# Optimization experiments

Hardware: AMD Instinct MI355X
Metric: run time of the kernel (lower is better)

The kernel has to match this reference:

```python
import jax, jax.numpy as jnp
import numpy as np
import math

# dims
B, T, HFEAT, E = 32, 8, 128, 128
NUM_CLS, NUM_GLOBAL = 4, 2
NSP = NUM_CLS + NUM_GLOBAL            # 6 special tokens
SCALES = (1, 4, 8)
WINDOW = 4
NHEAD = 8
DH = E // NHEAD                        # 16
NLAYERS = 2                            # blocks per scale = ceil(6/3)
NS = len(SCALES)
F = 512                                # dim_feedforward
ROPE_BASE = 100000.0
NEG = -1e9


def setup_inputs() -> dict:
    key = jax.random.key(0)
    ks = jax.random.split(key, 16)
    def rn(k, shape, s=0.02):
        return jax.random.normal(k, shape, jnp.float32) * s
    inp = {
        'embeddings': jax.random.normal(ks[0], (B, T, NSP + HFEAT, E), jnp.float32),
        'cls_tokens': rn(ks[1], (NUM_CLS, E)),
        'global_tokens': rn(ks[2], (NUM_GLOBAL, E)),
        'Wq': rn(ks[3], (NS, NLAYERS, E, E)),
        'bq': jnp.zeros((NS, NLAYERS, E), jnp.float32),
        'Wk': rn(ks[4], (NS, NLAYERS, E, E)),
        'bk': jnp.zeros((NS, NLAYERS, E), jnp.float32),
        'Wv': rn(ks[5], (NS, NLAYERS, E, E)),
        'bv': jnp.zeros((NS, NLAYERS, E), jnp.float32),
        'Wo': rn(ks[6], (NS, NLAYERS, E, E)),
        'bo': jnp.zeros((NS, NLAYERS, E), jnp.float32),
        'ln1_g': jnp.ones((NS, NLAYERS, E), jnp.float32),
        'ln1_b': jnp.zeros((NS, NLAYERS, E), jnp.float32),
        'ln2_g': jnp.ones((NS, NLAYERS, E), jnp.float32),
        'ln2_b': jnp.zeros((NS, NLAYERS, E), jnp.float32),
        'W1': rn(ks[7], (NS, NLAYERS, E, F)),
        'b1': jnp.zeros((NS, NLAYERS, F), jnp.float32),
        'W2': rn(ks[8], (NS, NLAYERS, F, E)),
        'b2': jnp.zeros((NS, NLAYERS, E), jnp.float32),
        'out_g': jnp.ones((E,), jnp.float32),
        'out_b': jnp.zeros((E,), jnp.float32),
    }
    return inp


def _layernorm(x, g, b, eps=1e-5):
    mu = x.mean(-1, keepdims=True)
    var = ((x - mu) ** 2).mean(-1, keepdims=True)
    return (x - mu) * jax.lax.rsqrt(var + eps) * g + b


def _rope(x):
    # x: (BT, L, H, DH); rotate-half RoPE over head dim
    L = x.shape[1]
    half = DH // 2
    inv = ROPE_BASE ** (-jnp.arange(half, dtype=jnp.float32) / half)
    ang = jnp.arange(L, dtype=jnp.float32)[:, None] * inv[None, :]   # (L, half)
    cos = jnp.cos(ang)[None, :, None, :]
    sin = jnp.sin(ang)[None, :, None, :]
    x1, x2 = x[..., :half], x[..., half:]
    return jnp.concatenate([x1 * cos - x2 * sin, x1 * sin + x2 * cos], axis=-1)


def _sparse_bias(L):
    # global(first NSP) rows/cols fully connected, others window +-WINDOW, diag allowed
    i = jnp.arange(L)
    allowed = (jnp.abs(i[:, None] - i[None, :]) <= WINDOW) | (i[:, None] < NSP) | (i[None, :] < NSP)
    return jnp.where(allowed, 0.0, NEG).astype(jnp.float32)  # (L, L) additive


def _encoder(x, s, Wq, bq, Wk, bk, Wv, bv, Wo, bo, ln1_g, ln1_b, ln2_g, ln2_b, W1, b1, W2, b2, bias):
    # x: (BT, L, E); pre-norm transformer encoder with RoPE attention
    BT, L, _ = x.shape
    for l in range(NLAYERS):
        h = _layernorm(x, ln1_g[s, l], ln1_b[s, l])
        q = (h @ Wq[s, l] + bq[s, l]).reshape(BT, L, NHEAD, DH)
        k = (h @ Wk[s, l] + bk[s, l]).reshape(BT, L, NHEAD, DH)
        v = (h @ Wv[s, l] + bv[s, l]).reshape(BT, L, NHEAD, DH)
        q, k = _rope(q), _rope(k)
        scores = jnp.einsum('blhd,bmhd->bhlm', q, k) / math.sqrt(DH) + bias[None, None]
        attn = jax.nn.softmax(scores, axis=-1)
        o = jnp.einsum('bhlm,bmhd->blhd', attn, v).reshape(BT, L, E)
        x = x + o @ Wo[s, l] + bo[s, l]
        h2 = _layernorm(x, ln2_g[s, l], ln2_b[s, l])
        x = x + jax.nn.gelu(h2 @ W1[s, l] + b1[s, l]) @ W2[s, l] + b2[s, l]
    return x


def reference(embeddings, cls_tokens, global_tokens, Wq, bq, Wk, bk, Wv, bv, Wo, bo,
              ln1_g, ln1_b, ln2_g, ln2_b, W1, b1, W2, b2, out_g, out_b):
    Bb, Tt, HC, Ee = embeddings.shape
    feats = embeddings[..., NSP:, :]                                 # (B,T,H,E)
    specials = jnp.broadcast_to(
        jnp.concatenate([cls_tokens, global_tokens], axis=0)[None, None],
        (Bb, Tt, NSP, Ee))
    cls_per_scale = []
    for s, g in enumerate(SCALES):
        H = feats.shape[2]
        K = H // g  # H divisible by all scales
        grouped = feats.reshape(Bb, Tt, K, g, Ee).mean(axis=3)       # contiguous mean grouping
        seq = jnp.concatenate([specials, grouped], axis=2)           # (B,T,L,E)
        L = NSP + K
        x = seq.reshape(Bb * Tt, L, Ee)
        bias = _sparse_bias(L)
        out = _encoder(x, s, Wq, bq, Wk, bk, Wv, bv, Wo, bo,
                       ln1_g, ln1_b, ln2_g, ln2_b, W1, b1, W2, b2, bias)
        cls_per_scale.append(out.reshape(Bb, Tt, L, Ee)[..., :NUM_CLS, :])
    cls_out = jnp.stack(cls_per_scale, axis=0).mean(axis=0)          # (B,T,num_cls,E)
    cls_out = _layernorm(cls_out, out_g, out_b)
    return cls_out.reshape(Bb, Tt, NUM_CLS * Ee)
```

## Files before the change

kernel.cpp:

```cpp
#include <hip/hip_runtime.h>
#include <hip/hip_bf16.h>

#define BT     256
#define EDIM   128
#define NSP    6
#define RT     49664
#define O1     34304
#define O2     44032
#define KSTR   20

typedef unsigned short u16;
typedef short s16x8 __attribute__((ext_vector_type(8)));
typedef float f32x4 __attribute__((ext_vector_type(4)));

__device__ __forceinline__ float u2f(u16 u){ union{unsigned i; float f;} v; v.i=((unsigned)u)<<16; return v.f; }
__device__ __forceinline__ u16 f2u(float f){
  union{float f; unsigned i;} v; v.f = f;
  unsigned r = v.i + 0x7FFF + ((v.i >> 16) & 1);
  return (u16)(r >> 16);
}
__device__ __forceinline__ float ldin(const void* p, size_t idx, int flag){
  return flag ? u2f(((const u16*)p)[idx]) : ((const float*)p)[idx];
}
__device__ __forceinline__ void unp8(uint4 v, float* f){
  f[0]=u2f((u16)(v.x)); f[1]=u2f((u16)(v.x>>16));
  f[2]=u2f((u16)(v.y)); f[3]=u2f((u16)(v.y>>16));
  f[4]=u2f((u16)(v.z)); f[5]=u2f((u16)(v.z>>16));
  f[6]=u2f((u16)(v.w)); f[7]=u2f((u16)(v.w>>16));
}

__device__ __forceinline__ void rowinfo(int row, int& s, int& r, int& L, int& g){
  if (row < O1){ s=0; r=row;    L=134; g=1; }
  else if (row < O2){ s=1; r=row-O1; L=38; g=4; }
  else { s=2; r=row-O2; L=22; g=8; }
}

__device__ __forceinline__ float gelu_f(float x){
  float u = x*(1.5957691216f + 0.0713548162f*x*x);
  return x * __builtin_amdgcn_rcpf(1.f + __expf(-u));
}

__global__ void detect_k(const void* ln1g, int* flagp){
  unsigned v = *(const unsigned*)ln1g;
  *flagp = (v == 0x3F803F80u) ? 1 : 0;
}

struct CArg { const void* src; unsigned dstoff; unsigned n; unsigned inblk; unsigned outblk; };
struct CArgs { CArg a[12]; };
__global__ __launch_bounds__(256) void conv_k(CArgs ca, u16* stage, const int* flagp){
  int i = blockIdx.y;
  int flag = *flagp;
  const CArg& c = ca.a[i];
  for (unsigned idx = blockIdx.x*256u + threadIdx.x; idx < c.n; idx += gridDim.x*256u){
    unsigned blk = idx / c.inblk, r = idx % c.inblk;
    float v = flag ? u2f(((const u16*)c.src)[idx]) : ((const float*)c.src)[idx];
    stage[c.dstoff + blk*c.outblk + r] = flag ? ((const u16*)c.src)[idx] : f2u(v);
  }
}

__global__ __launch_bounds__(256) void convw_k(const void* s0, const void* s1, const void* s2,
                                               u16* dst, int K, int N, int Nsrc, const int* flagp)
{
  int flag = *flagp;
  const void* srcs[3] = {s0, s1, s2};
  int total = 6 * K * N;
  for (int idx = blockIdx.x*256 + threadIdx.x; idx < total; idx += gridDim.x*256) {
    int blk = idx / (K*N);
    int rem = idx % (K*N);
    int j = rem & 7;
    int t = rem >> 3;
    int n = t % N;
    int ck = t / N;
    int k = ck*8 + j;
    int w = n / Nsrc;
    int nn = n - w*Nsrc;
    size_t sidx = (size_t)blk*K*Nsrc + (size_t)k*Nsrc + nn;
    dst[idx] = flag ? ((const u16*)srcs[w])[sidx] : f2u(((const float*)srcs[w])[sidx]);
  }
}

__global__ __launch_bounds__(128) void build_k(const void* __restrict__ emb,
                                               const void* __restrict__ cls,
                                               const void* __restrict__ glob,
                                               float* __restrict__ x,
                                               u16* __restrict__ H,
                                               const u16* __restrict__ lnG,
                                               const u16* __restrict__ lnB,
                                               const int* flagp)
{
  __shared__ float red[4];
  int flag = *flagp;
  int row = blockIdx.x, e = threadIdx.x;
  int s, r, L, g; rowinfo(row, s, r, L, g);
  int seq = r / L, pos = r % L;
  float val;
  if (pos < NSP) {
    val = (pos < 4) ? ldin(cls, pos*EDIM + e, flag) : ldin(glob, (pos-4)*EDIM + e, flag);
  } else {
    int k = pos - NSP;
    size_t base = ((size_t)seq*134 + NSP + (size_t)k*g)*EDIM + e;
    float sum = 0.f;
    for (int j = 0; j < g; j++) sum += ldin(emb, base + (size_t)j*EDIM, flag);
    val = sum / (float)g;
  }
  x[(size_t)row*EDIM + e] = val;
  int wid = e >> 6;
  float sum = val, ss = val*val;
  #pragma unroll
  for (int off = 32; off; off >>= 1) { sum += __shfl_xor(sum, off); ss += __shfl_xor(ss, off); }
  if ((e & 63) == 0) { red[wid] = sum; red[2+wid] = ss; }
  __syncthreads();
  float ts = red[0]+red[1], tss = red[2]+red[3];
  float mu = ts * (1.f/128.f);
  float var = tss * (1.f/128.f) - mu*mu;
  float rs = rsqrtf(var + 1e-5f);
  const u16* gp = lnG + s*2*EDIM;
  const u16* bp = lnB + s*2*EDIM;
  H[(size_t)row*EDIM + e] = f2u((val-mu)*rs*u2f(gp[e]) + u2f(bp[e]));
}

template<int EPI>
__global__ __launch_bounds__(256) void gemm64_k(
    const u16* __restrict__ A,
    const u16* __restrict__ Wt, const u16* __restrict__ Bias,
    u16* __restrict__ C, int ldc, int N, int layer,
    float* __restrict__ X, u16* __restrict__ H,
    const u16* __restrict__ lnG, const u16* __restrict__ lnB, int lnidx)
{
  __shared__ u16 As[4][16*136];
  __shared__ u16 Bs[16*128*8];
  const int row0 = blockIdx.x * 64;
  const int n0 = blockIdx.y * 128;
  const int s = row0 < O1 ? 0 : (row0 < O2 ? 1 : 2);
  const u16* Wp = Wt + (size_t)(s*2+layer)*128*N;
  const u16* bp = Bias + (size_t)(s*2+layer)*N + n0;
  const int tid = threadIdx.x;
  const int lane = tid & 63, w = tid >> 6;
  const int g = lane >> 4, l15 = lane & 15;

  #pragma unroll
  for (int i = 0; i < 4; i++) {
    int unit = lane + i*64;
    int r = unit >> 4, kc = unit & 15;
    *(uint4*)&As[w][r*136 + kc*8] = *(const uint4*)(A + (size_t)(row0 + w*16 + r)*128 + kc*8);
  }
  #pragma unroll
  for (int i = 0; i < 8; i++) {
    int u = tid + i*256;
    int kb = u >> 7, nn = u & 127;
    *(uint4*)&Bs[u*8] = *(const uint4*)(Wp + ((size_t)kb*N + n0 + nn)*8);
  }
  __syncthreads();

  f32x4 acc[8];
  #pragma unroll
  for (int nt = 0; nt < 8; nt++) acc[nt] = (f32x4){0.f,0.f,0.f,0.f};
  #pragma unroll
  for (int ks = 0; ks < 4; ks++) {
    int c = ks*4 + g;
    s16x8 af = *(const s16x8*)&As[w][l15*136 + c*8];
    #pragma unroll
    for (int nt = 0; nt < 8; nt++) {
      s16x8 bf = *(const s16x8*)&Bs[(c*128 + nt*16 + l15)*8];
      acc[nt] = __builtin_amdgcn_mfma_f32_16x16x32_bf16(af, bf, acc[nt], 0, 0, 0);
    }
  }

  float bb[8];
  #pragma unroll
  for (int nt = 0; nt < 8; nt++) bb[nt] = u2f(bp[nt*16 + l15]);

  #pragma unroll
  for (int reg = 0; reg < 4; reg++) {
    int row = row0 + w*16 + g*4 + reg;
    #pragma unroll
    for (int nt = 0; nt < 8; nt++)
      C[(size_t)row*ldc + n0 + nt*16 + l15] = f2u(acc[nt][reg] + bb[nt]);
  }
}

template<int LNFUSE>
__global__ __launch_bounds__(256, 3) void woffn_k(
    const u16* __restrict__ A,
    const u16* __restrict__ Wot, const u16* __restrict__ Bo,
    const u16* __restrict__ W1t, const u16* __restrict__ B1,
    const u16* __restrict__ W2t, const u16* __restrict__ B2,
    float* __restrict__ X,
    u16* __restrict__ H,
    const u16* __restrict__ ln2G, const u16* __restrict__ ln2B,
    const u16* __restrict__ ln1G, const u16* __restrict__ ln1B,
    int layer)
{
  __shared__ u16 Hs[4][16*136];
  __shared__ u16 Ts[2][4][16*40];
  const int row0 = blockIdx.x * 64;
  const int s = row0 < O1 ? 0 : (row0 < O2 ? 1 : 2);
  const int sl = s*2 + layer;
  const u16* Wop = Wot + (size_t)sl*16384;
  const u16* bop = Bo  + sl*128;
  const u16* W1p = W1t + (size_t)sl*65536;
  const u16* b1p = B1  + sl*512;
  const u16* W2p = W2t + (size_t)sl*65536;
  const u16* b2p = B2  + sl*128;
  const int tid = threadIdx.x;
  const int lane = tid & 63, w = tid >> 6;
  const int g = lane >> 4, l15 = lane & 15;

  s16x8 af[4];
  {
    const u16* arow = A + (size_t)(row0 + w*16 + l15)*128;
    #pragma unroll
    for (int ks = 0; ks < 4; ks++) af[ks] = *(const s16x8*)(arow + (ks*4 + g)*8);
  }
  const u16* wobase = Wop + ((size_t)g*128 + l15)*8;

  f32x4 acc2[8];
  #pragma unroll
  for (int nt = 0; nt < 8; nt++) acc2[nt] = (f32x4){0.f,0.f,0.f,0.f};
  #pragma unroll
  for (int ks = 0; ks < 4; ks++) {
    s16x8 bw[8];
    #pragma unroll
    for (int nt = 0; nt < 8; nt++)
      bw[nt] = *(const s16x8*)(wobase + ((size_t)ks*4096 + nt*128));
    #pragma unroll
    for (int nt = 0; nt < 8; nt++)
      acc2[nt] = __builtin_amdgcn_mfma_f32_16x16x32_bf16(af[ks], bw[nt], acc2[nt], 0, 0, 0);
  }

  {
    float gam[8], bet[8], bo_[8];
    const u16* gp  = ln2G + sl*EDIM;
    const u16* bp2 = ln2B + sl*EDIM;
    #pragma unroll
    for (int nt = 0; nt < 8; nt++) {
      gam[nt] = u2f(gp[nt*16+l15]); bet[nt] = u2f(bp2[nt*16+l15]);
      bo_[nt] = u2f(bop[nt*16+l15]);
    }
    #pragma unroll
    for (int reg = 0; reg < 4; reg++) {
      int row = row0 + w*16 + g*4 + reg;
      float vals[8], ps = 0.f, pss = 0.f;
      #pragma unroll
      for (int nt = 0; nt < 8; nt++) {
        float v = acc2[nt][reg] + bo_[nt] + X[(size_t)row*128 + nt*16 + l15];
        vals[nt] = v; ps += v; pss += v*v;
      }
      #pragma unroll
      for (int off = 1; off < 16; off <<= 1) { ps += __shfl_xor(ps, off); pss += __shfl_xor(pss, off); }
      float mu = ps * (1.f/128.f);
      float var = pss * (1.f/128.f) - mu*mu;
      float rs = rsqrtf(var + 1e-5f);
      #pragma unroll
      for (int nt = 0; nt < 8; nt++) {
        acc2[nt][reg] = vals[nt];
        Hs[w][(g*4+reg)*136 + nt*16 + l15] = f2u((vals[nt]-mu)*rs*gam[nt] + bet[nt]);
      }
    }
  }

  s16x8 hf[4];
  #pragma unroll
  for (int ks = 0; ks < 4; ks++) hf[ks] = *(const s16x8*)&Hs[w][l15*136 + (ks*4+g)*8];

  const u16* w1base = W1p + ((size_t)g*512 + l15)*8;
  const u16* w2base = W2p + ((size_t)g*128 + l15)*8;

  s16x8 bw1[8];
  #pragma unroll
  for (int ks = 0; ks < 4; ks++)
    #pragma unroll
    for (int nt = 0; nt < 2; nt++)
      bw1[ks*2+nt] = *(const s16x8*)(w1base + (size_t)(ks*2048 + nt*16)*8);

  {
    f32x4 acc1[2];
    acc1[0] = (f32x4){0.f,0.f,0.f,0.f};
    acc1[1] = (f32x4){0.f,0.f,0.f,0.f};
    #pragma unroll
    for (int ks = 0; ks < 4; ks++) {
      acc1[0] = __builtin_amdgcn_mfma_f32_16x16x32_bf16(hf[ks], bw1[ks*2+0], acc1[0], 0, 0, 0);
      acc1[1] = __builtin_amdgcn_mfma_f32_16x16x32_bf16(hf[ks], bw1[ks*2+1], acc1[1], 0, 0, 0);
    }
    #pragma unroll
    for (int ks = 0; ks < 4; ks++)
      #pragma unroll
      for (int nt = 0; nt < 2; nt++)
        bw1[ks*2+nt] = *(const s16x8*)(w1base + (size_t)(ks*2048 + 32 + nt*16)*8);
    #pragma unroll
    for (int nt = 0; nt < 2; nt++) {
      float bb1 = u2f(b1p[nt*16 + l15]);
      #pragma unroll
      for (int reg = 0; reg < 4; reg++)
        Ts[0][w][(g*4+reg)*40 + nt*16 + l15] = f2u(gelu_f(acc1[nt][reg] + bb1));
    }
  }

  for (int i = 1; i < 16; i++) {
    const int f0 = i*32, fp = f0 - 32;
    u16* tsC = &Ts[i & 1][w][0];
    const u16* tsP = &Ts[(i & 1) ^ 1][w][0];

    s16x8 bw2a[4];
    #pragma unroll
    for (int nt = 0; nt < 4; nt++)
      bw2a[nt] = *(const s16x8*)(w2base + (size_t)(fp*16 + nt*16)*8);
    s16x8 af2p = *(const s16x8*)(tsP + l15*40 + g*8);

    f32x4 acc1[2];
    acc1[0] = (f32x4){0.f,0.f,0.f,0.f};
    acc1[1] = (f32x4){0.f,0.f,0.f,0.f};
    #pragma unroll
    for (int ks = 0; ks < 4; ks++) {
      acc1[0] = __builtin_amdgcn_mfma_f32_16x16x32_bf16(hf[ks], bw1[ks*2+0], acc1[0], 0, 0, 0);
      acc1[1] = __builtin_amdgcn_mfma_f32_16x16x32_bf16(hf[ks], bw1[ks*2+1], acc1[1], 0, 0, 0);
    }
    {
      const int fn = (f0 + 32) & 511;
      #pragma unroll
      for (int ks = 0; ks < 4; ks++)
        #pragma unroll
        for (int nt = 0; nt < 2; nt++)
          bw1[ks*2+nt] = *(const s16x8*)(w1base + (size_t)(ks*2048 + fn + nt*16)*8);
    }
    s16x8 bw2b[4];
    #pragma unroll
    for (int nt = 0; nt < 4; nt++)
      bw2b[nt] = *(const s16x8*)(w2base + (size_t)(fp*16 + 64 + nt*16)*8);

    #pragma unroll
    for (int nt = 0; nt < 2; nt++) {
      float bb1 = u2f(b1p[f0 + nt*16 + l15]);
      #pragma unroll
      for (int reg = 0; reg < 4; reg++)
        tsC[(g*4+reg)*40 + nt*16 + l15] = f2u(gelu_f(acc1[nt][reg] + bb1));
    }

    #pragma unroll
    for (int nt = 0; nt < 4; nt++)
      acc2[nt] = __builtin_amdgcn_mfma_f32_16x16x32_bf16(af2p, bw2a[nt], acc2[nt], 0, 0, 0);
    #pragma unroll
    for (int nt = 0; nt < 4; nt++)
      acc2[4+nt] = __builtin_amdgcn_mfma_f32_16x16x32_bf16(af2p, bw2b[nt], acc2[4+nt], 0, 0, 0);
  }

  {
    s16x8 af2p = *(const s16x8*)&Ts[1][w][l15*40 + g*8];
    #pragma unroll
    for (int nt = 0; nt < 8; nt++) {
      s16x8 b = *(const s16x8*)(w2base + (size_t)(480*16 + nt*16)*8);
      acc2[nt] = __builtin_amdgcn_mfma_f32_16x16x32_bf16(af2p, b, acc2[nt], 0, 0, 0);
    }
  }

  float bb2[8];
  #pragma unroll
  for (int nt = 0; nt < 8; nt++) bb2[nt] = u2f(b2p[nt*16 + l15]);

  if (LNFUSE) {
    float gam[8], bet[8];
    const u16* gp  = ln1G + (s*2+1)*EDIM;
    const u16* bpn = ln1B + (s*2+1)*EDIM;
    #pragma unroll
    for (int nt = 0; nt < 8; nt++) { gam[nt] = u2f(gp[nt*16+l15]); bet[nt] = u2f(bpn[nt*16+l15]); }
    #pragma unroll
    for (int reg = 0; reg < 4; reg++) {
      int row = row0 + w*16 + g*4 + reg;
      float vals[8], ps = 0.f, pss = 0.f;
      #pragma unroll
      for (int nt = 0; nt < 8; nt++) {
        float v = acc2[nt][reg] + bb2[nt];
        vals[nt] = v; ps += v; pss += v*v;
      }
      #pragma unroll
      for (int off = 1; off < 16; off <<= 1) { ps += __shfl_xor(ps, off); pss += __shfl_xor(pss, off); }
      float mu = ps * (1.f/128.f);
      float var = pss * (1.f/128.f) - mu*mu;
      float rs = rsqrtf(var + 1e-5f);
      #pragma unroll
      for (int nt = 0; nt < 8; nt++) {
        size_t cidx = (size_t)row*128 + nt*16 + l15;
        X[cidx] = vals[nt];
        H[cidx] = f2u((vals[nt]-mu)*rs*gam[nt] + bet[nt]);
      }
    }
  } else {
    #pragma unroll
    for (int reg = 0; reg < 4; reg++) {
      int row = row0 + w*16 + g*4 + reg;
      #pragma unroll
      for (int nt = 0; nt < 8; nt++) {
        size_t cidx = (size_t)row*128 + nt*16 + l15;
        X[cidx] = acc2[nt][reg] + bb2[nt];
      }
    }
  }
}

__global__ __launch_bounds__(128) void attn_k(const u16* __restrict__ qkv, u16* __restrict__ o)
{
  __shared__ float Ks[134*KSTR];
  __shared__ float Vs[134*KSTR];
  int gseq = blockIdx.x, hd = blockIdx.y;
  int L, base;
  if (gseq < 256)      { L = 134; base = gseq*134; }
  else if (gseq < 512) { L = 38;  base = O1 + (gseq-256)*38; }
  else                 { L = 22;  base = O2 + (gseq-512)*22; }
  int tid = threadIdx.x;
  for (int u = tid; u < L*2; u += 128) {
    int kv = u & 1, row = u >> 1;
    const u16* p = qkv + (size_t)(base+row)*384 + 128 + kv*128 + hd*16;
    uint4 w0 = *(const uint4*)p, w1 = *(const uint4*)(p+8);
    float f[16];
    unp8(w0, f); unp8(w1, f+8);
    if (kv == 0) {
      #pragma unroll
      for (int d = 0; d < 8; d++) {
        float inv = __expf(-(float)d * (11.512925465f/8.f));
        float ang = (float)row * inv;
        float cs = __cosf(ang), sn = __sinf(ang);
        float a = f[d], b = f[d+8];
        f[d]   = a*cs - b*sn;
        f[d+8] = a*sn + b*cs;
      }
    }
    float* dst = (kv ? Vs : Ks) + row*KSTR;
    #pragma unroll
    for (int d = 0; d < 16; d++) dst[d] = f[d];
  }
  __syncthreads();

  for (int it = tid; it < L - NSP; it += 128) {
    int row = NSP + it;
    const u16* qp = qkv + (size_t)(base+row)*384 + hd*16;
    uint4 w0 = *(const uint4*)qp, w1 = *(const uint4*)(qp+8);
    float q[16]; unp8(w0, q); unp8(w1, q+8);
    #pragma unroll
    for (int d = 0; d < 8; d++) {
      float inv = __expf(-(float)d * (11.512925465f/8.f));
      float ang = (float)row * inv;
      float cs = __cosf(ang), sn = __sinf(ang);
      float a = q[d], b = q[d+8];
      q[d]   = a*cs - b*sn;
      q[d+8] = a*sn + b*cs;
    }
    float m = -1e30f, l = 0.f, oa[16] = {};
    auto step = [&](int j){
      const float4* kr = (const float4*)(Ks + j*KSTR);
      float4 k0 = kr[0], k1 = kr[1], k2 = kr[2], k3 = kr[3];
      float sc = q[0]*k0.x + q[1]*k0.y + q[2]*k0.z + q[3]*k0.w
               + q[4]*k1.x + q[5]*k1.y + q[6]*k1.z + q[7]*k1.w
               + q[8]*k2.x + q[9]*k2.y + q[10]*k2.z + q[11]*k2.w
               + q[12]*k3.x + q[13]*k3.y + q[14]*k3.z + q[15]*k3.w;
      sc *= 0.25f;
      float nm = fmaxf(m, sc);
      float scale = __expf(m - nm);
      float pexp = __expf(sc - nm);
      l = l*scale + pexp;
      const float4* vr = (const float4*)(Vs + j*KSTR);
      float4 v0 = vr[0], v1 = vr[1], v2 = vr[2], v3 = vr[3];
      oa[0]=oa[0]*scale+pexp*v0.x;  oa[1]=oa[1]*scale+pexp*v0.y;
      oa[2]=oa[2]*scale+pexp*v0.z;  oa[3]=oa[3]*scale+pexp*v0.w;
      oa[4]=oa[4]*scale+pexp*v1.x;  oa[5]=oa[5]*scale+pexp*v1.y;
      oa[6]=oa[6]*scale+pexp*v1.z;  oa[7]=oa[7]*scale+pexp*v1.w;
      oa[8]=oa[8]*scale+pexp*v2.x;  oa[9]=oa[9]*scale+pexp*v2.y;
      oa[10]=oa[10]*scale+pexp*v2.z; oa[11]=oa[11]*scale+pexp*v2.w;
      oa[12]=oa[12]*scale+pexp*v3.x; oa[13]=oa[13]*scale+pexp*v3.y;
      oa[14]=oa[14]*scale+pexp*v3.z; oa[15]=oa[15]*scale+pexp*v3.w;
      m = nm;
    };
    #pragma unroll
    for (int j = 0; j < NSP; j++) step(j);
    int jlo = (row-4 > NSP) ? row-4 : NSP;
    int jhi = (row+4 < L-1) ? row+4 : L-1;
    for (int j = jlo; j <= jhi; j++) step(j);
    float invl = 1.f/l;
    u16* op = o + (size_t)(base+row)*EDIM + hd*16;
    #pragma unroll
    for (int d = 0; d < 16; d++) op[d] = f2u(oa[d]*invl);
  }

  if (tid < 96) {
    int row = tid >> 4;
    int u = tid & 15;
    const u16* qp = qkv + (size_t)(base+row)*384 + hd*16;
    uint4 w0 = *(const uint4*)qp, w1 = *(const uint4*)(qp+8);
    float q[16]; unp8(w0, q); unp8(w1, q+8);
    #pragma unroll
    for (int d = 0; d < 8; d++) {
      float inv = __expf(-(float)d * (11.512925465f/8.f));
      float ang = (float)row * inv;
      float cs = __cosf(ang), sn = __sinf(ang);
      float a = q[d], b = q[d+8];
      q[d]   = a*cs - b*sn;
      q[d+8] = a*sn + b*cs;
    }
    float m = -1e30f, l = 0.f, oa[16] = {};
    for (int j = u; j < L; j += 16) {
      const float4* kr = (const float4*)(Ks + j*KSTR);
      float4 k0 = kr[0], k1 = kr[1], k2 = kr[2], k3 = kr[3];
      float sc = q[0]*k0.x + q[1]*k0.y + q[2]*k0.z + q[3]*k0.w
               + q[4]*k1.x + q[5]*k1.y + q[6]*k1.z + q[7]*k1.w
               + q[8]*k2.x + q[9]*k2.y + q[10]*k2.z + q[11]*k2.w
               + q[12]*k3.x + q[13]*k3.y + q[14]*k3.z + q[15]*k3.w;
      sc *= 0.25f;
      float nm = fmaxf(m, sc);
      float scale = __expf(m - nm);
      float pexp = __expf(sc - nm);
      l = l*scale + pexp;
      const float4* vr = (const float4*)(Vs + j*KSTR);
      float4 v0 = vr[0], v1 = vr[1], v2 = vr[2], v3 = vr[3];
      oa[0]=oa[0]*scale+pexp*v0.x;  oa[1]=oa[1]*scale+pexp*v0.y;
      oa[2]=oa[2]*scale+pexp*v0.z;  oa[3]=oa[3]*scale+pexp*v0.w;
      oa[4]=oa[4]*scale+pexp*v1.x;  oa[5]=oa[5]*scale+pexp*v1.y;
      oa[6]=oa[6]*scale+pexp*v1.z;  oa[7]=oa[7]*scale+pexp*v1.w;
      oa[8]=oa[8]*scale+pexp*v2.x;  oa[9]=oa[9]*scale+pexp*v2.y;
      oa[10]=oa[10]*scale+pexp*v2.z; oa[11]=oa[11]*scale+pexp*v2.w;
      oa[12]=oa[12]*scale+pexp*v3.x; oa[13]=oa[13]*scale+pexp*v3.y;
      oa[14]=oa[14]*scale+pexp*v3.z; oa[15]=oa[15]*scale+pexp*v3.w;
      m = nm;
    }
    #pragma unroll
    for (int off = 1; off < 16; off <<= 1) {
      float m2 = __shfl_xor(m, off);
      float l2 = __shfl_xor(l, off);
      float nm = fmaxf(m, m2);
      float s1 = __expf(m - nm), s2 = __expf(m2 - nm);
      #pragma unroll
      for (int d = 0; d < 16; d++) {
        float o2 = __shfl_xor(oa[d], off);
        oa[d] = oa[d]*s1 + o2*s2;
      }
      l = l*s1 + l2*s2;
      m = nm;
    }
    if (u == 0) {
      float invl = 1.f/l;
      u16* op = o + (size_t)(base+row)*EDIM + hd*16;
      #pragma unroll
      for (int d = 0; d < 16; d++) op[d] = f2u(oa[d]*invl);
    }
  }
}

__global__ __launch_bounds__(256) void final_k(const float* __restrict__ x,
                                               const u16* __restrict__ G,
                                               const u16* __restrict__ Bt,
                                               void* __restrict__ out, const int* flagp)
{
  int flag = *flagp;
  int wid = threadIdx.x >> 6, lane = threadIdx.x & 63;
  int idx = blockIdx.x*4 + wid;
  int seq = idx >> 2, c = idx & 3;
  size_t r0 = ((size_t)seq*134 + c)*EDIM;
  size_t r1 = ((size_t)O1 + (size_t)seq*38 + c)*EDIM;
  size_t r2 = ((size_t)O2 + (size_t)seq*22 + c)*EDIM;
  float v0 = (x[r0+lane]    + x[r1+lane]    + x[r2+lane])    * (1.f/3.f);
  float v1 = (x[r0+64+lane] + x[r1+64+lane] + x[r2+64+lane]) * (1.f/3.f);
  float sum = v0 + v1;
  #pragma unroll
  for (int off = 32; off; off >>= 1) sum += __shfl_xor(sum, off);
  float mu = sum * (1.f/128.f);
  float d0 = v0 - mu, d1 = v1 - mu;
  float var = d0*d0 + d1*d1;
  #pragma unroll
  for (int off = 32; off; off >>= 1) var += __shfl_xor(var, off);
  var *= (1.f/128.f);
  float rs = rsqrtf(var + 1e-5f);
  float o0 = d0*rs*u2f(G[lane])    + u2f(Bt[lane]);
  float o1 = d1*rs*u2f(G[64+lane]) + u2f(Bt[64+lane]);
  size_t oi0 = (size_t)seq*512 + c*128 + lane;
  if (flag) { ((u16*)out)[oi0] = f2u(o0); ((u16*)out)[oi0+64] = f2u(o1); }
  else      { ((float*)out)[oi0] = o0;    ((float*)out)[oi0+64] = o1; }
}

#define S_WQKV 0u
#define S_BQKV 294912u
#define S_WO   297216u
#define S_BO   395520u
#define S_W1   396288u
#define S_B1   789504u
#define S_W2   792576u
#define S_B2   1185792u
#define S_L1G  1186560u
#define S_L1B  1187328u
#define S_L2G  1188096u
#define S_L2B  1188864u
#define S_OG   1189632u
#define S_OB   1189760u

extern "C" void kernel_launch(void* const* d_in, const int* in_sizes, int n_in,
                              void* d_out, int out_size, void* d_ws, size_t ws_size,
                              hipStream_t stream) {
  char* wsb = (char*)d_ws;
  int*   flagp = (int*)wsb;
  u16*   stage = (u16*)(wsb + 64);
  float* x     = (float*)(wsb + (size_t)2379840);
  u16*   h     = (u16*)(wsb + (size_t)27807808);
  u16*   qkv   = (u16*)(wsb + (size_t)40521792);

  detect_k<<<1, 1, 0, stream>>>(d_in[11], flagp);

  CArgs ca;
  CArg list[12] = {
    { d_in[4],  S_BQKV,       768, 128, 384 },
    { d_in[6],  S_BQKV+128u,  768, 128, 384 },
    { d_in[8],  S_BQKV+256u,  768, 128, 384 },
    { d_in[10], S_BO,         768, 128, 128 },
    { d_in[16], S_B1,        3072, 512, 512 },
    { d_in[18], S_B2,         768, 128, 128 },
    { d_in[11], S_L1G,        768, 128, 128 },
    { d_in[12], S_L1B,        768, 128, 128 },
    { d_in[13], S_L2G,        768, 128, 128 },
    { d_in[14], S_L2B,        768, 128, 128 },
    { d_in[19], S_OG,         128, 128, 128 },
    { d_in[20], S_OB,         128, 128, 128 },
  };
  for (int i = 0; i < 12; i++) ca.a[i] = list[i];
  conv_k<<<dim3(4, 12), 256, 0, stream>>>(ca, stage, flagp);

  convw_k<<<256, 256, 0, stream>>>(d_in[3], d_in[5], d_in[7], stage+S_WQKV, 128, 384, 128, flagp);
  convw_k<<<128, 256, 0, stream>>>(d_in[9], d_in[9], d_in[9], stage+S_WO,   128, 128, 128, flagp);
  convw_k<<<256, 256, 0, stream>>>(d_in[15],d_in[15],d_in[15],stage+S_W1,   128, 512, 512, flagp);
  convw_k<<<256, 256, 0, stream>>>(d_in[17],d_in[17],d_in[17],stage+S_W2,   512, 128, 128, flagp);

  build_k<<<RT, 128, 0, stream>>>(d_in[0], d_in[1], d_in[2], x, h, stage+S_L1G, stage+S_L1B, flagp);

  for (int l = 0; l < 2; l++) {
    gemm64_k<0><<<dim3(RT/64, 3), 256, 0, stream>>>(h, stage+S_WQKV, stage+S_BQKV, qkv, 384, 384, l,
                                                    nullptr, nullptr, nullptr, nullptr, 0);
    attn_k<<<dim3(768, 8), 128, 0, stream>>>(qkv, h);
    if (l == 0)
      woffn_k<1><<<RT/64, 256, 0, stream>>>(h, stage+S_WO, stage+S_BO,
                                            stage+S_W1, stage+S_B1, stage+S_W2, stage+S_B2,
                                            x, h, stage+S_L2G, stage+S_L2B,
                                            stage+S_L1G, stage+S_L1B, 0);
    else
      woffn_k<0><<<RT/64, 256, 0, stream>>>(h, stage+S_WO, stage+S_BO,
                                            stage+S_W1, stage+S_B1, stage+S_W2, stage+S_B2,
                                            x, nullptr, stage+S_L2G, stage+S_L2B,
                                            stage+S_L1G, stage+S_L1B, 1);
  }
  final_k<<<BT, 256, 0, stream>>>(x, stage+S_OG, stage+S_OB, d_out, flagp);
}
```

Measured before the change: 363.3 us.

## Split FFN hidden dim across wave pairs and drop LDS staging in QKV GEMM

The fused Wo+FFN kernel now handles 32 rows per block, with two waves per 16-row tile that each take half of the 512-wide FFN hidden dimension. The partial W2 accumulators are reduced through shared memory before the LN epilogue. This doubles the grid and cuts the serial per-wave FFN chain, at the cost of an extra LDS reduction, two block barriers, and redundant Wo work being skipped by the second wave. Separately, the QKV GEMM loads A and weight fragments straight from global memory into registers instead of staging them in LDS. Both kernels get a minimum of 4 blocks per CU in their launch bounds.

```diff
diff --git a/kernel.cpp b/kernel.cpp
--- a/kernel.cpp
+++ b/kernel.cpp
@@ -119,68 +119,57 @@
   H[(size_t)row*EDIM + e] = f2u((val-mu)*rs*u2f(gp[e]) + u2f(bp[e]));
 }
 
-template<int EPI>
-__global__ __launch_bounds__(256) void gemm64_k(
+__global__ __launch_bounds__(256, 4) void qkv_k(
     const u16* __restrict__ A,
     const u16* __restrict__ Wt, const u16* __restrict__ Bias,
-    u16* __restrict__ C, int ldc, int N, int layer,
-    float* __restrict__ X, u16* __restrict__ H,
-    const u16* __restrict__ lnG, const u16* __restrict__ lnB, int lnidx)
+    u16* __restrict__ C, int layer)
 {
-  __shared__ u16 As[4][16*136];
-  __shared__ u16 Bs[16*128*8];
   const int row0 = blockIdx.x * 64;
   const int n0 = blockIdx.y * 128;
   const int s = row0 < O1 ? 0 : (row0 < O2 ? 1 : 2);
-  const u16* Wp = Wt + (size_t)(s*2+layer)*128*N;
-  const u16* bp = Bias + (size_t)(s*2+layer)*N + n0;
+  const int sl = s*2 + layer;
+  const u16* Wp = Wt + (size_t)sl*49152;
+  const u16* bp = Bias + (size_t)sl*384 + n0;
   const int tid = threadIdx.x;
   const int lane = tid & 63, w = tid >> 6;
   const int g = lane >> 4, l15 = lane & 15;
 
-  #pragma unroll
-  for (int i = 0; i < 4; i++) {
-    int unit = lane + i*64;
-    int r = unit >> 4, kc = unit & 15;
-    *(uint4*)&As[w][r*136 + kc*8] = *(const uint4*)(A + (size_t)(row0 + w*16 + r)*128 + kc*8);
-  }
-  #pragma unroll
-  for (int i = 0; i < 8; i++) {
-    int u = tid + i*256;
-    int kb = u >> 7, nn = u & 127;
-    *(uint4*)&Bs[u*8] = *(const uint4*)(Wp + ((size_t)kb*N + n0 + nn)*8);
-  }
-  __syncthreads();
+  s16x8 af[4];
+  {
+    const u16* arow = A + (size_t)(row0 + w*16 + l15)*128;
+    #pragma unroll
+    for (int ks = 0; ks < 4; ks++) af[ks] = *(const s16x8*)(arow + (ks*4 + g)*8);
+  }
+  const u16* wbase = Wp + ((size_t)g*384 + n0 + l15)*8;
 
   f32x4 acc[8];
   #pragma unroll
   for (int nt = 0; nt < 8; nt++) acc[nt] = (f32x4){0.f,0.f,0.f,0.f};
   #pragma unroll
   for (int ks = 0; ks < 4; ks++) {
-    int c = ks*4 + g;
-    s16x8 af = *(const s16x8*)&As[w][l15*136 + c*8];
-    #pragma unroll
-    for (int nt = 0; nt < 8; nt++) {
-      s16x8 bf = *(const s16x8*)&Bs[(c*128 + nt*16 + l15)*8];
-      acc[nt] = __builtin_amdgcn_mfma_f32_16x16x32_bf16(af, bf, acc[nt], 0, 0, 0);
-    }
+    s16x8 bw[8];
+    #pragma unroll
+    for (int nt = 0; nt < 8; nt++)
+      bw[nt] = *(const s16x8*)(wbase + (size_t)ks*12288 + nt*128);
+    #pragma unroll
+    for (int nt = 0; nt < 8; nt++)
+      acc[nt] = __builtin_amdgcn_mfma_f32_16x16x32_bf16(af[ks], bw[nt], acc[nt], 0, 0, 0);
   }
 
   float bb[8];
   #pragma unroll
   for (int nt = 0; nt < 8; nt++) bb[nt] = u2f(bp[nt*16 + l15]);
-
   #pragma unroll
   for (int reg = 0; reg < 4; reg++) {
     int row = row0 + w*16 + g*4 + reg;
     #pragma unroll
     for (int nt = 0; nt < 8; nt++)
-      C[(size_t)row*ldc + n0 + nt*16 + l15] = f2u(acc[nt][reg] + bb[nt]);
+      C[(size_t)row*384 + n0 + nt*16 + l15] = f2u(acc[nt][reg] + bb[nt]);
   }
 }
 
 template<int LNFUSE>
-__global__ __launch_bounds__(256, 3) void woffn_k(
+__global__ __launch_bounds__(256, 4) void woffn_k(
     const u16* __restrict__ A,
     const u16* __restrict__ Wot, const u16* __restrict__ Bo,
     const u16* __restrict__ W1t, const u16* __restrict__ B1,
@@ -191,10 +180,15 @@
     const u16* __restrict__ ln1G, const u16* __restrict__ ln1B,
     int layer)
 {
-  __shared__ u16 Hs[4][16*136];
-  __shared__ u16 Ts[2][4][16*40];
-  const int row0 = blockIdx.x * 64;
-  const int s = row0 < O1 ? 0 : (row0 < O2 ? 1 : 2);
+  __shared__ u16 Hs[2][16*136];
+  __shared__ u16 Ts[4][2][16*40];
+  __shared__ f32x4 Pacc[2][512];
+  const int tid = threadIdx.x;
+  const int lane = tid & 63, w = tid >> 6;
+  const int tile = w >> 1, roleB = w & 1;
+  const int g = lane >> 4, l15 = lane & 15;
+  const int trow0 = blockIdx.x*32 + tile*16;
+  const int s = trow0 < O1 ? 0 : (trow0 < O2 ? 1 : 2);
   const int sl = s*2 + layer;
   const u16* Wop = Wot + (size_t)sl*16384;
   const u16* bop = Bo  + sl*128;
@@ -202,33 +196,29 @@
   const u16* b1p = B1  + sl*512;
   const u16* W2p = W2t + (size_t)sl*65536;
   const u16* b2p = B2  + sl*128;
-  const int tid = threadIdx.x;
-  const int lane = tid & 63, w = tid >> 6;
-  const int g = lane >> 4, l15 = lane & 15;
-
-  s16x8 af[4];
-  {
-    const u16* arow = A + (size_t)(row0 + w*16 + l15)*128;
-    #pragma unroll
-    for (int ks = 0; ks < 4; ks++) af[ks] = *(const s16x8*)(arow + (ks*4 + g)*8);
-  }
-  const u16* wobase = Wop + ((size_t)g*128 + l15)*8;
 
   f32x4 acc2[8];
   #pragma unroll
   for (int nt = 0; nt < 8; nt++) acc2[nt] = (f32x4){0.f,0.f,0.f,0.f};
-  #pragma unroll
-  for (int ks = 0; ks < 4; ks++) {
-    s16x8 bw[8];
-    #pragma unroll
-    for (int nt = 0; nt < 8; nt++)
-      bw[nt] = *(const s16x8*)(wobase + ((size_t)ks*4096 + nt*128));
-    #pragma unroll
-    for (int nt = 0; nt < 8; nt++)
-      acc2[nt] = __builtin_amdgcn_mfma_f32_16x16x32_bf16(af[ks], bw[nt], acc2[nt], 0, 0, 0);
-  }
-
-  {
+
+  if (!roleB) {
+    s16x8 af[4];
+    {
+      const u16* arow = A + (size_t)(trow0 + l15)*128;
+      #pragma unroll
+      for (int ks = 0; ks < 4; ks++) af[ks] = *(const s16x8*)(arow + (ks*4 + g)*8);
+    }
+    const u16* wobase = Wop + ((size_t)g*128 + l15)*8;
+    #pragma unroll
+    for (int ks = 0; ks < 4; ks++) {
+      s16x8 bw[8];
+      #pragma unroll
+      for (int nt = 0; nt < 8; nt++)
+        bw[nt] = *(const s16x8*)(wobase + ((size_t)ks*4096 + nt*128));
+      #pragma unroll
+      for (int nt = 0; nt < 8; nt++)
+        acc2[nt] = __builtin_amdgcn_mfma_f32_16x16x32_bf16(af[ks], bw[nt], acc2[nt], 0, 0, 0);
+    }
     float gam[8], bet[8], bo_[8];
     const u16* gp  = ln2G + sl*EDIM;
     const u16* bp2 = ln2B + sl*EDIM;
@@ -239,7 +229,7 @@
     }
     #pragma unroll
     for (int reg = 0; reg < 4; reg++) {
-      int row = row0 + w*16 + g*4 + reg;
+      int row = trow0 + g*4 + reg;
       float vals[8], ps = 0.f, pss = 0.f;
       #pragma unroll
       for (int nt = 0; nt < 8; nt++) {
@@ -254,24 +244,26 @@
       #pragma unroll
       for (int nt = 0; nt < 8; nt++) {
         acc2[nt][reg] = vals[nt];
-        Hs[w][(g*4+reg)*136 + nt*16 + l15] = f2u((vals[nt]-mu)*rs*gam[nt] + bet[nt]);
+        Hs[tile][(g*4+reg)*136 + nt*16 + l15] = f2u((vals[nt]-mu)*rs*gam[nt] + bet[nt]);
       }
     }
   }
 
-  s16x8 hf[4];
-  #pragma unroll
-  for (int ks = 0; ks < 4; ks++) hf[ks] = *(const s16x8*)&Hs[w][l15*136 + (ks*4+g)*8];
-
+  const int fbase = roleB ? 256 : 0;
   const u16* w1base = W1p + ((size_t)g*512 + l15)*8;
   const u16* w2base = W2p + ((size_t)g*128 + l15)*8;
-
   s16x8 bw1[8];
   #pragma unroll
   for (int ks = 0; ks < 4; ks++)
     #pragma unroll
     for (int nt = 0; nt < 2; nt++)
-      bw1[ks*2+nt] = *(const s16x8*)(w1base + (size_t)(ks*2048 + nt*16)*8);
+      bw1[ks*2+nt] = *(const s16x8*)(w1base + (size_t)(ks*2048 + fbase + nt*16)*8);
+
+  __syncthreads();
+
+  s16x8 hf[4];
+  #pragma unroll
+  for (int ks = 0; ks < 4; ks++) hf[ks] = *(const s16x8*)&Hs[tile][l15*136 + (ks*4+g)*8];
 
   {
     f32x4 acc1[2];
@@ -286,20 +278,20 @@
     for (int ks = 0; ks < 4; ks++)
       #pragma unroll
       for (int nt = 0; nt < 2; nt++)
-        bw1[ks*2+nt] = *(const s16x8*)(w1base + (size_t)(ks*2048 + 32 + nt*16)*8);
+        bw1[ks*2+nt] = *(const s16x8*)(w1base + (size_t)(ks*2048 + fbase + 32 + nt*16)*8);
     #pragma unroll
     for (int nt = 0; nt < 2; nt++) {
-      float bb1 = u2f(b1p[nt*16 + l15]);
+      float bb1 = u2f(b1p[fbase + nt*16 + l15]);
       #pragma unroll
       for (int reg = 0; reg < 4; reg++)
-        Ts[0][w][(g*4+reg)*40 + nt*16 + l15] = f2u(gelu_f(acc1[nt][reg] + bb1));
-    }
-  }
-
-  for (int i = 1; i < 16; i++) {
-    const int f0 = i*32, fp = f0 - 32;
-    u16* tsC = &Ts[i & 1][w][0];
-    const u16* tsP = &Ts[(i & 1) ^ 1][w][0];
+        Ts[w][0][(g*4+reg)*40 + nt*16 + l15] = f2u(gelu_f(acc1[nt][reg] + bb1));
+    }
+  }
+
+  for (int i = 1; i < 8; i++) {
+    const int f0 = fbase + i*32, fp = f0 - 32;
+    u16* tsC = &Ts[w][i & 1][0];
+    const u16* tsP = &Ts[w][(i & 1) ^ 1][0];
 
     s16x8 bw2a[4];
     #pragma unroll
@@ -345,13 +337,24 @@
   }
 
   {
-    s16x8 af2p = *(const s16x8*)&Ts[1][w][l15*40 + g*8];
+    const int fp = fbase + 224;
+    s16x8 af2p = *(const s16x8*)&Ts[w][1][l15*40 + g*8];
     #pragma unroll
     for (int nt = 0; nt < 8; nt++) {
-      s16x8 b = *(const s16x8*)(w2base + (size_t)(480*16 + nt*16)*8);
+      s16x8 b = *(const s16x8*)(w2base + (size_t)(fp*16 + nt*16)*8);
       acc2[nt] = __builtin_amdgcn_mfma_f32_16x16x32_bf16(af2p, b, acc2[nt], 0, 0, 0);
     }
   }
+
+  if (roleB) {
+    #pragma unroll
+    for (int j = 0; j < 8; j++) Pacc[tile][j*64 + lane] = acc2[j];
+  }
+  __syncthreads();
+  if (roleB) return;
+
+  #pragma unroll
+  for (int j = 0; j < 8; j++) acc2[j] += Pacc[tile][j*64 + lane];
 
   float bb2[8];
   #pragma unroll
@@ -365,7 +368,7 @@
     for (int nt = 0; nt < 8; nt++) { gam[nt] = u2f(gp[nt*16+l15]); bet[nt] = u2f(bpn[nt*16+l15]); }
     #pragma unroll
     for (int reg = 0; reg < 4; reg++) {
-      int row = row0 + w*16 + g*4 + reg;
+      int row = trow0 + g*4 + reg;
       float vals[8], ps = 0.f, pss = 0.f;
       #pragma unroll
       for (int nt = 0; nt < 8; nt++) {
@@ -387,7 +390,7 @@
   } else {
     #pragma unroll
     for (int reg = 0; reg < 4; reg++) {
-      int row = row0 + w*16 + g*4 + reg;
+      int row = trow0 + g*4 + reg;
       #pragma unroll
       for (int nt = 0; nt < 8; nt++) {
         size_t cidx = (size_t)row*128 + nt*16 + l15;
@@ -627,16 +630,15 @@
   build_k<<<RT, 128, 0, stream>>>(d_in[0], d_in[1], d_in[2], x, h, stage+S_L1G, stage+S_L1B, flagp);
 
   for (int l = 0; l < 2; l++) {
-    gemm64_k<0><<<dim3(RT/64, 3), 256, 0, stream>>>(h, stage+S_WQKV, stage+S_BQKV, qkv, 384, 384, l,
-                                                    nullptr, nullptr, nullptr, nullptr, 0);
+    qkv_k<<<dim3(RT/64, 3), 256, 0, stream>>>(h, stage+S_WQKV, stage+S_BQKV, qkv, l);
     attn_k<<<dim3(768, 8), 128, 0, stream>>>(qkv, h);
     if (l == 0)
-      woffn_k<1><<<RT/64, 256, 0, stream>>>(h, stage+S_WO, stage+S_BO,
+      woffn_k<1><<<RT/32, 256, 0, stream>>>(h, stage+S_WO, stage+S_BO,
                                             stage+S_W1, stage+S_B1, stage+S_W2, stage+S_B2,
                                             x, h, stage+S_L2G, stage+S_L2B,
                                             stage+S_L1G, stage+S_L1B, 0);
     else
-      woffn_k<0><<<RT/64, 256, 0, stream>>>(h, stage+S_WO, stage+S_BO,
+      woffn_k<0><<<RT/32, 256, 0, stream>>>(h, stage+S_WO, stage+S_BO,
                                             stage+S_W1, stage+S_B1, stage+S_W2, stage+S_B2,
                                             x, nullptr, stage+S_L2G, stage+S_L2B,
                                             stage+S_L1G, stage+S_L1B, 1);
```

After: 401.0 us. 10.4% more time.
